# Performance work log

Hardware: AMD Instinct MI355X
Metric: run time of the kernel (lower is better)

Reference implementation:

```python
import jax, jax.numpy as jnp
import numpy as np

LOW_RANK = 8   # q passed to torch.svd_lowrank
NITER = 2      # torch.svd_lowrank default power-iteration count


def setup_inputs() -> dict:
    key = jax.random.key(0)
    k1, k2 = jax.random.split(key)
    x = jax.random.normal(k1, (32, 256, 56, 56), dtype=jnp.float32)
    # Gaussian test matrix used by torch.svd_lowrank's range finder on A^T:
    # R = randn(A.mT.shape[-1]=C, q), shared across the (H*W) batch.
    omega = jax.random.normal(k2, (256, LOW_RANK), dtype=jnp.float32)
    return {"x": x, "omega": omega}


def _qr_q(a):
    # reduced QR, batched over leading dims; inputs are tall (m >= n)
    return jnp.linalg.qr(a, mode="reduced")[0]


def reference(x, omega):
    B, C, H, W = x.shape
    # [B,C,H,W] -> [H,W,C,B] -> (H*W, C, B): H*W small matrices A of shape (C, B)
    A = jnp.transpose(x, (2, 3, 1, 0)).reshape(H * W, C, B)

    # torch.svd_lowrank with n=B > q takes the transposed branch:
    #   Q = get_approximate_basis(A^T, q, niter=2)   (Q: (B, q), orthonormal cols)
    #   U S V^T == (A @ Q) @ Q^T  -> reconstruction is A Q Q^T
    Y = jnp.einsum("mcb,cq->mbq", A, omega)      # A^T @ Omega : (M, B, q)
    Q = _qr_q(Y)
    for _ in range(NITER):
        Z = jnp.einsum("mcb,mbq->mcq", A, Q)     # A @ Q       : (M, C, q)
        Qc = _qr_q(Z)
        Y = jnp.einsum("mcb,mcq->mbq", A, Qc)    # A^T @ Qc    : (M, B, q)
        Q = _qr_q(Y)

    P = jnp.einsum("mcb,mbq->mcq", A, Q)         # A @ Q       : (M, C, q)
    y = jnp.einsum("mcq,mbq->mcb", P, Q)         # A Q Q^T     : (M, C, B)

    y = y.reshape(H, W, C, B)
    return jnp.transpose(y, (3, 2, 0, 1))        # back to [B, C, H, W]
```

## Files before the change

### kernel.cpp

```cpp
#include <hip/hip_runtime.h>
#include <math.h>

#define HW   3136
#define NB   32
#define NC   256
#define TM   16
#define CC   8
#define LDP  36
#define SLABC (TM * LDP)
#define SLABF (CC * SLABC)

#define NS   4
#define CSL  (NC / NS)
#define NCH  (CSL / CC)
#define GK   1280

#define YT_(mi,b,q) Sm[(mi)*265 + (q)*33 + (b)]
#define WT_(mi,b,q) Sm[4240 + (mi)*265 + (q)*33 + (b)]
#define SS_(mi,k)   Sm[8480 + (mi)*65 + (k)]
#define SMEMF 9520

__host__ __device__ constexpr int TRI(int i, int j) { return i*8 - (i*(i+1))/2 + j; }

__device__ __forceinline__ void stage_load512(float4* r, const float* __restrict__ xg,
                                              int c0, int m0, int t) {
#pragma unroll
  for (int i = 0; i < 2; ++i) {
    int id = t + i * 512;
    int cc = id >> 7, b = (id >> 2) & 31, mq = id & 3;
    r[i] = *reinterpret_cast<const float4*>(
        xg + (size_t)(b * NC + c0 + cc) * HW + m0 + mq * 4);
  }
}
__device__ __forceinline__ void stage_write_t(const float4* r, float* sl, int t) {
#pragma unroll
  for (int i = 0; i < 2; ++i) {
    int id = t + i * 512;
    int cc = id >> 7, b = (id >> 2) & 31, mq = id & 3;
    float* p = sl + cc * SLABC + (mq * 4) * LDP + b;
    p[0 * LDP] = r[i].x;
    p[1 * LDP] = r[i].y;
    p[2 * LDP] = r[i].z;
    p[3 * LDP] = r[i].w;
  }
}

__device__ __forceinline__ void chol8(const float* __restrict__ Sm, int mi, float* Rl) {
#pragma unroll
  for (int i = 0; i < 8; ++i) {
    float d = SS_(mi, i * 8 + i);
#pragma unroll
    for (int k = 0; k < 8; ++k) {
      if (k < i) { float rk = Rl[TRI(k, i)]; d = fmaf(-rk, rk, d); }
    }
    float rii = sqrtf(fmaxf(d, 1e-30f));
    float inv = 1.0f / rii;
    Rl[TRI(i, i)] = inv;
#pragma unroll
    for (int j = 0; j < 8; ++j) {
      if (j > i) {
        float v = SS_(mi, i * 8 + j);
#pragma unroll
        for (int k = 0; k < 8; ++k) {
          if (k < i) v = fmaf(-Rl[TRI(k, i)], Rl[TRI(k, j)], v);
        }
        Rl[TRI(i, j)] = v * inv;
      }
    }
  }
}

__device__ __forceinline__ void trsm1row(const float* __restrict__ srcB, float* __restrict__ dstB,
                                         int mi, int r, const float* Rl) {
  float yv[8], qv[8];
#pragma unroll
  for (int q = 0; q < 8; ++q) yv[q] = srcB[mi * 265 + q * 33 + r];
#pragma unroll
  for (int j = 0; j < 8; ++j) {
    float a = yv[j];
#pragma unroll
    for (int k = 0; k < 8; ++k) {
      if (k < j) a = fmaf(-qv[k], Rl[TRI(k, j)], a);
    }
    qv[j] = a * Rl[TRI(j, j)];
  }
#pragma unroll
  for (int q = 0; q < 8; ++q) dstB[mi * 265 + q * 33 + r] = qv[q];
}

__device__ __forceinline__ void cholqr32(float* __restrict__ Sm, int mi, int r) {
#pragma unroll
  for (int e = 0; e < 2; ++e) {
    int idx = r + e * 32, i = idx >> 3, j = idx & 7;
    float s = 0.f;
#pragma unroll
    for (int b = 0; b < 32; ++b) s = fmaf(YT_(mi, b, i), YT_(mi, b, j), s);
    SS_(mi, idx) = s;
  }
  __syncthreads();
  float Rl[36];
  chol8(Sm, mi, Rl);
  trsm1row(Sm, Sm, mi, r, Rl);
  __syncthreads();
}

__global__ __launch_bounds__(512, 4) void tsvd_k1a(const float* __restrict__ x,
                                                   const float* __restrict__ omega,
                                                   float* __restrict__ Gp) {
  __shared__ float Sm[2 * SLABF];
  const int t = threadIdx.x;
  const int mi = t & 15, r = t >> 4;
  const int s = blockIdx.x & (NS - 1);
  const int mt = blockIdx.x / NS;
  const int m0 = mt * TM, m = m0 + mi;
  const int c0 = s * CSL;

  float G[32], Y[8];
#pragma unroll
  for (int b = 0; b < 32; ++b) G[b] = 0.f;
#pragma unroll
  for (int q = 0; q < 8; ++q) Y[q] = 0.f;

  float4 st[2];
  stage_load512(st, x, c0, m0, t);
  stage_write_t(st, Sm, t);
  for (int ch = 0; ch < NCH; ++ch) {
    if (ch + 1 < NCH) stage_load512(st, x, c0 + (ch + 1) * CC, m0, t);
    __syncthreads();
    const float* cur = Sm + (ch & 1) * SLABF;
#pragma unroll
    for (int cc = 0; cc < CC; ++cc) {
      const int c = c0 + ch * CC + cc;
      const float* v = cur + cc * SLABC + mi * LDP;
      const float ar = v[r];
#pragma unroll
      for (int k = 0; k < 8; ++k) {
        float4 vb = *reinterpret_cast<const float4*>(v + 4 * k);
        G[4 * k + 0] = fmaf(ar, vb.x, G[4 * k + 0]);
        G[4 * k + 1] = fmaf(ar, vb.y, G[4 * k + 1]);
        G[4 * k + 2] = fmaf(ar, vb.z, G[4 * k + 2]);
        G[4 * k + 3] = fmaf(ar, vb.w, G[4 * k + 3]);
      }
#pragma unroll
      for (int q = 0; q < 8; ++q) Y[q] = fmaf(ar, omega[c * 8 + q], Y[q]);
    }
    if (ch + 1 < NCH) stage_write_t(st, Sm + ((ch + 1) & 1) * SLABF, t);
  }

  const size_t sb = (size_t)s * GK;
#pragma unroll
  for (int b = 0; b < 32; ++b)
    Gp[(sb + r * 32 + b) * HW + m] = G[b];
#pragma unroll
  for (int q = 0; q < 8; ++q)
    Gp[(sb + 1024 + r * 8 + q) * HW + m] = Y[q];
}

__global__ __launch_bounds__(256, 2) void tsvd_k1b(const float* __restrict__ Gp,
                                                   float* __restrict__ Mws) {
  __shared__ float Sm[SMEMF];
  const int t = threadIdx.x;
  const int r = t & 31, mi = t >> 5;
  const int m0 = blockIdx.x * 8, m = m0 + mi;

  float G0[32], Y0[8];
#pragma unroll
  for (int b = 0; b < 32; ++b) {
    float a = 0.f;
#pragma unroll
    for (int s = 0; s < NS; ++s) a += Gp[((size_t)s * GK + r * 32 + b) * HW + m];
    G0[b] = a;
  }
#pragma unroll
  for (int q = 0; q < 8; ++q) {
    float a = 0.f;
#pragma unroll
    for (int s = 0; s < NS; ++s) a += Gp[((size_t)s * GK + 1024 + r * 8 + q) * HW + m];
    Y0[q] = a;
  }

#pragma unroll
  for (int q = 0; q < 8; ++q) YT_(mi, r, q) = Y0[q];
  __syncthreads();

#pragma unroll
  for (int it = 0; it < 3; ++it) {
    cholqr32(Sm, mi, r);
    cholqr32(Sm, mi, r);
    if (it < 2) {
      float u[8];
#pragma unroll
      for (int q = 0; q < 8; ++q) {
        float a = 0.f;
#pragma unroll
        for (int b = 0; b < 32; ++b) a = fmaf(G0[b], YT_(mi, b, q), a);
        u[q] = a;
      }
#pragma unroll
      for (int q = 0; q < 8; ++q) WT_(mi, r, q) = u[q];
      __syncthreads();
#pragma unroll
      for (int e = 0; e < 2; ++e) {
        int idx = r + e * 32, i2 = idx >> 3, j2 = idx & 7;
        float a = 0.f;
#pragma unroll
        for (int b = 0; b < 32; ++b) a = fmaf(YT_(mi, b, i2), WT_(mi, b, j2), a);
        SS_(mi, idx) = a;
      }
      __syncthreads();
      {
        float Rl[36];
        chol8(Sm, mi, Rl);
        trsm1row(Sm, Sm + 4240, mi, r, Rl);
      }
      __syncthreads();
#pragma unroll
      for (int q = 0; q < 8; ++q) {
        float a = 0.f;
#pragma unroll
        for (int b = 0; b < 32; ++b) a = fmaf(G0[b], WT_(mi, b, q), a);
        u[q] = a;
      }
#pragma unroll
      for (int q = 0; q < 8; ++q) YT_(mi, r, q) = u[q];
      __syncthreads();
    }
  }

  float q0[8];
#pragma unroll
  for (int q = 0; q < 8; ++q) q0[q] = YT_(mi, r, q);
#pragma unroll
  for (int b2 = 0; b2 < 32; ++b2) {
    float a = 0.f;
#pragma unroll
    for (int q = 0; q < 8; ++q) a = fmaf(q0[q], YT_(mi, b2, q), a);
    Mws[(size_t)(r * 32 + b2) * HW + m] = a;
  }
}

__global__ __launch_bounds__(512, 4) void tsvd_k2(const float* __restrict__ x,
                                                  const float* __restrict__ Mws,
                                                  float* __restrict__ y) {
  __shared__ float Sm[2 * SLABF];
  const int t = threadIdx.x;
  const int mi = t & 15, r = t >> 4;
  const int bid = blockIdx.x;
  const int mt = bid % 196, cq = bid / 196;
  const int m0 = mt * TM, m = m0 + mi;
  const int cbase = cq * 32;

  float Mc[32];
#pragma unroll
  for (int b = 0; b < 32; ++b)
    Mc[b] = Mws[(size_t)(b * 32 + r) * HW + m];

  float4 st[2];
  stage_load512(st, x, cbase, m0, t);
  stage_write_t(st, Sm, t);
  for (int ch = 0; ch < 4; ++ch) {
    if (ch + 1 < 4) stage_load512(st, x, cbase + (ch + 1) * CC, m0, t);
    __syncthreads();
    const float* cur = Sm + (ch & 1) * SLABF;
#pragma unroll
    for (int cc = 0; cc < CC; ++cc) {
      const int c = cbase + ch * CC + cc;
      const float* v = cur + cc * SLABC + mi * LDP;
      float a = 0.f;
#pragma unroll
      for (int k = 0; k < 8; ++k) {
        float4 vb = *reinterpret_cast<const float4*>(v + 4 * k);
        a = fmaf(vb.x, Mc[4 * k + 0], a);
        a = fmaf(vb.y, Mc[4 * k + 1], a);
        a = fmaf(vb.z, Mc[4 * k + 2], a);
        a = fmaf(vb.w, Mc[4 * k + 3], a);
      }
      y[((size_t)r * NC + c) * HW + m] = a;
    }
    if (ch + 1 < 4) stage_write_t(st, Sm + ((ch + 1) & 1) * SLABF, t);
  }
}

extern "C" void kernel_launch(void* const* d_in, const int* in_sizes, int n_in,
                              void* d_out, int out_size, void* d_ws, size_t ws_size,
                              hipStream_t stream) {
  const float* x     = (const float*)d_in[0];
  const float* omega = (const float*)d_in[1];
  float* y   = (float*)d_out;
  float* Mws = (float*)d_ws;
  float* Gp  = (float*)d_out;

  tsvd_k1a<<<196 * NS, 512, 0, stream>>>(x, omega, Gp);
  tsvd_k1b<<<HW / 8, 256, 0, stream>>>(Gp, Mws);
  tsvd_k2<<<196 * 8, 512, 0, stream>>>(x, Mws, y);
}
```

Baseline: 358.4 us.

## Store partial Gram and projector workspaces as per-pixel contiguous float4 records

The partial Gram/Y buffer and the final 32x32 projector buffer change from a pixel-minor layout to a contiguous record per pixel. Each thread now reads and writes 128-byte contiguous chunks with float4 accesses. This is aimed mainly at the reduction/QR kernel, whose old reads and writes used strides of whole HW planes across lanes. In exchange, lanes with neighbouring pixels in k1a and k2 now touch addresses several KB apart instead of adjacent words. The minimum-blocks hint on the middle kernel is also dropped.

```diff
diff --git a/kernel.cpp b/kernel.cpp
--- a/kernel.cpp
+++ b/kernel.cpp
@@ -147,17 +147,16 @@
     if (ch + 1 < NCH) stage_write_t(st, Sm + ((ch + 1) & 1) * SLABF, t);
   }
 
-  const size_t sb = (size_t)s * GK;
-#pragma unroll
-  for (int b = 0; b < 32; ++b)
-    Gp[(sb + r * 32 + b) * HW + m] = G[b];
-#pragma unroll
-  for (int q = 0; q < 8; ++q)
-    Gp[(sb + 1024 + r * 8 + q) * HW + m] = Y[q];
-}
-
-__global__ __launch_bounds__(256, 2) void tsvd_k1b(const float* __restrict__ Gp,
-                                                   float* __restrict__ Mws) {
+  float4* rec = reinterpret_cast<float4*>(Gp + ((size_t)s * HW + m) * GK);
+#pragma unroll
+  for (int k = 0; k < 8; ++k)
+    rec[r * 8 + k] = make_float4(G[4 * k + 0], G[4 * k + 1], G[4 * k + 2], G[4 * k + 3]);
+  rec[256 + r * 2 + 0] = make_float4(Y[0], Y[1], Y[2], Y[3]);
+  rec[256 + r * 2 + 1] = make_float4(Y[4], Y[5], Y[6], Y[7]);
+}
+
+__global__ __launch_bounds__(256) void tsvd_k1b(const float* __restrict__ Gp,
+                                                float* __restrict__ Mws) {
   __shared__ float Sm[SMEMF];
   const int t = threadIdx.x;
   const int r = t & 31, mi = t >> 5;
@@ -165,18 +164,24 @@
 
   float G0[32], Y0[8];
 #pragma unroll
-  for (int b = 0; b < 32; ++b) {
-    float a = 0.f;
-#pragma unroll
-    for (int s = 0; s < NS; ++s) a += Gp[((size_t)s * GK + r * 32 + b) * HW + m];
-    G0[b] = a;
-  }
-#pragma unroll
-  for (int q = 0; q < 8; ++q) {
-    float a = 0.f;
-#pragma unroll
-    for (int s = 0; s < NS; ++s) a += Gp[((size_t)s * GK + 1024 + r * 8 + q) * HW + m];
-    Y0[q] = a;
+  for (int b = 0; b < 32; ++b) G0[b] = 0.f;
+#pragma unroll
+  for (int q = 0; q < 8; ++q) Y0[q] = 0.f;
+#pragma unroll
+  for (int s = 0; s < NS; ++s) {
+    const float4* rec = reinterpret_cast<const float4*>(Gp + ((size_t)s * HW + m) * GK);
+#pragma unroll
+    for (int k = 0; k < 8; ++k) {
+      float4 v = rec[r * 8 + k];
+      G0[4 * k + 0] += v.x;
+      G0[4 * k + 1] += v.y;
+      G0[4 * k + 2] += v.z;
+      G0[4 * k + 3] += v.w;
+    }
+    float4 y0 = rec[256 + r * 2 + 0];
+    float4 y1 = rec[256 + r * 2 + 1];
+    Y0[0] += y0.x; Y0[1] += y0.y; Y0[2] += y0.z; Y0[3] += y0.w;
+    Y0[4] += y1.x; Y0[5] += y1.y; Y0[6] += y1.z; Y0[7] += y1.w;
   }
 
 #pragma unroll
@@ -230,12 +235,19 @@
   float q0[8];
 #pragma unroll
   for (int q = 0; q < 8; ++q) q0[q] = YT_(mi, r, q);
-#pragma unroll
-  for (int b2 = 0; b2 < 32; ++b2) {
-    float a = 0.f;
-#pragma unroll
-    for (int q = 0; q < 8; ++q) a = fmaf(q0[q], YT_(mi, b2, q), a);
-    Mws[(size_t)(r * 32 + b2) * HW + m] = a;
+  float4* mrec = reinterpret_cast<float4*>(Mws + (size_t)m * 1024);
+#pragma unroll
+  for (int bq = 0; bq < 8; ++bq) {
+    float a[4];
+#pragma unroll
+    for (int e = 0; e < 4; ++e) {
+      int b2 = bq * 4 + e;
+      float acc = 0.f;
+#pragma unroll
+      for (int q = 0; q < 8; ++q) acc = fmaf(q0[q], YT_(mi, b2, q), acc);
+      a[e] = acc;
+    }
+    mrec[r * 8 + bq] = make_float4(a[0], a[1], a[2], a[3]);
   }
 }
 
@@ -251,9 +263,14 @@
   const int cbase = cq * 32;
 
   float Mc[32];
-#pragma unroll
-  for (int b = 0; b < 32; ++b)
-    Mc[b] = Mws[(size_t)(b * 32 + r) * HW + m];
+  {
+    const float4* mrec = reinterpret_cast<const float4*>(Mws + (size_t)m * 1024);
+#pragma unroll
+    for (int k = 0; k < 8; ++k) {
+      float4 v = mrec[r * 8 + k];
+      Mc[4 * k + 0] = v.x; Mc[4 * k + 1] = v.y; Mc[4 * k + 2] = v.z; Mc[4 * k + 3] = v.w;
+    }
+  }
 
   float4 st[2];
   stage_load512(st, x, cbase, m0, t);
```

New measurement: 316.3 us. 1.13x faster.
